# Kernel tuning notes

Measured on AMD Instinct MI355X. Metric: run time of the kernel, lower is better.

## Reference

```python
import jax, jax.numpy as jnp
import numpy as np

EPS = 1e-08
PARTIAL_NORM = 1.5
TOPK = 8
SELF_MOD_STEPS = 2


def _layernorm(x, g, b, eps=1e-05):
    mu = jnp.mean(x, axis=-1, keepdims=True)
    var = jnp.mean((x - mu) ** 2, axis=-1, keepdims=True)
    return (x - mu) / jnp.sqrt(var + eps) * g + b


def _spectral_normalize(w, iters=10):
    # mimic torch spectral_norm: divide by top singular value (power iteration)
    u = jnp.ones((w.shape[0],), w.dtype) / np.sqrt(w.shape[0])
    def step(u, _):
        v = w.T @ u
        v = v / (jnp.linalg.norm(v) + 1e-12)
        u2 = w @ v
        u2 = u2 / (jnp.linalg.norm(u2) + 1e-12)
        return u2, None
    u, _ = jax.lax.scan(step, u, None, length=iters)
    v = w.T @ u
    v = v / (jnp.linalg.norm(v) + 1e-12)
    sigma = u @ (w @ v)
    return w / sigma


def setup_inputs() -> dict:
    B, D, H, S, C = 8192, 2048, 1024, 3, 1000
    P = 1024  # proj_dim = ((max(H, D//2)+7)//8)*8
    key = jax.random.key(0)
    ks = jax.random.split(key, 16)
    x = jax.random.normal(ks[0], (B, D), jnp.float32)
    proj_w = jax.random.normal(ks[1], (P, D), jnp.float32) / np.sqrt(D)
    proj_b = jnp.zeros((P,), jnp.float32)
    ln_p_g = jnp.ones((P,), jnp.float32)
    ln_p_b = jnp.zeros((P,), jnp.float32)
    wf_w = jax.random.normal(ks[2], (S, 2 * H, P), jnp.float32) / np.sqrt(P)
    wf_w = jax.vmap(_spectral_normalize)(wf_w)
    wf_b = jax.random.normal(ks[3], (S, 2 * H), jnp.float32) * 0.02
    ln_g = jnp.ones((S, 2 * H), jnp.float32)
    ln_b = jnp.zeros((S, 2 * H), jnp.float32)
    temperature = jnp.ones((1,), jnp.float32)
    phases = jax.random.normal(ks[4], (S, 1), jnp.float32) * 0.5
    gate_w = jax.random.normal(ks[5], (H, H), jnp.float32) / np.sqrt(H)
    gate_b = jnp.zeros((H,), jnp.float32)
    cls_w1 = jax.random.normal(ks[6], (H, H), jnp.float32) / np.sqrt(H)
    cls_b1 = jnp.zeros((H,), jnp.float32)
    cls_w2 = jax.random.normal(ks[7], (C, H), jnp.float32) / np.sqrt(H)
    cls_b2 = jnp.zeros((C,), jnp.float32).at[1].set(0.75)
    return {"x": x, "proj_w": proj_w, "proj_b": proj_b, "ln_p_g": ln_p_g,
            "ln_p_b": ln_p_b, "wf_w": wf_w, "wf_b": wf_b, "ln_g": ln_g,
            "ln_b": ln_b, "temperature": temperature, "phases": phases,
            "gate_w": gate_w, "gate_b": gate_b, "cls_w1": cls_w1,
            "cls_b1": cls_b1, "cls_w2": cls_w2, "cls_b2": cls_b2}


def reference(x, proj_w, proj_b, ln_p_g, ln_p_b, wf_w, wf_b, ln_g, ln_b,
              temperature, phases, gate_w, gate_b, cls_w1, cls_b1, cls_w2, cls_b2):
    H = wf_w.shape[1] // 2
    # input projection (dropout is identity at eval)
    h = jax.nn.gelu(_layernorm(x @ proj_w.T + proj_b, ln_p_g, ln_p_b), approximate=False)
    # all wavefunctions at once: [B, S, 2H]
    out = jnp.einsum('bp,sep->bse', h, wf_w) + wf_b[None]
    out = _layernorm(out, ln_g[None], ln_b[None])
    out = jnp.exp(-out * out)  # ArcBell
    alpha, beta = out[..., :H], out[..., H:]
    norm_sq = jnp.sum(alpha ** 2 + beta ** 2, axis=-1, keepdims=True) + EPS
    factor = jnp.sqrt(PARTIAL_NORM ** 2 / norm_sq)
    alpha = alpha * factor
    beta = beta * factor
    phase = phases[None]  # [1, S, 1]
    c, s = jnp.cos(phase), jnp.sin(phase)
    wave_r = alpha * c - beta * s  # [B, S, H]
    wave_i = alpha * s + beta * c
    # cosine-similarity interference weights
    mean_real = jnp.mean(wave_r, axis=1)  # [B, H]
    mean_norm = jnp.sqrt(jnp.sum(mean_real ** 2, axis=-1, keepdims=True)) + EPS  # [B,1]
    wave_norms = jnp.sqrt(jnp.sum(wave_r ** 2, axis=-1, keepdims=True)) + EPS  # [B,S,1]
    dot = jnp.sum(wave_r * mean_real[:, None], axis=-1, keepdims=True)  # [B,S,1]
    cos_sim = (dot / (wave_norms * mean_norm[:, None]))[..., 0]  # [B,S]
    w = jax.nn.softmax(cos_sim / temperature, axis=1)[..., None]  # [B,S,1]
    sup_r = jnp.sum(wave_r * w, axis=1)  # [B,H]
    sup_i = jnp.sum(wave_i * w, axis=1)
    # self-modulation with leaky residual
    for _ in range(SELF_MOD_STEPS):
        mag = jnp.sqrt(sup_r ** 2 + sup_i ** 2 + EPS)
        gate = jax.nn.sigmoid(mag @ gate_w.T + gate_b)
        sup_r = sup_r * gate + sup_r * 0.1
        sup_i = sup_i * gate + sup_i * 0.1
    mag_sq = sup_r ** 2 + sup_i ** 2
    # top-k mask + scatter + renormalize
    _, inds = jax.lax.top_k(mag_sq, TOPK)
    rows = jnp.arange(mag_sq.shape[0])[:, None]
    mask = jnp.zeros_like(mag_sq).at[rows, inds].set(1.0)
    masked = mag_sq * mask
    probs = masked / (jnp.sum(masked, axis=-1, keepdims=True) + EPS)
    # classifier (dropout identity at eval)
    hid = jax.nn.gelu(probs @ cls_w1.T + cls_b1, approximate=False)
    logits = hid @ cls_w2.T + cls_b2
    return logits
```

## Files before the change

kernel.cpp:

```cpp
#include <hip/hip_runtime.h>
#include <cstdint>

typedef __attribute__((ext_vector_type(8))) __bf16 bf16x8;
typedef __attribute__((ext_vector_type(4))) __bf16 bf16x4;
typedef __attribute__((ext_vector_type(4))) float f32x4;
typedef unsigned long long u64;

__device__ __forceinline__ void gld_lds16(const void* g, void* l) {
  __builtin_amdgcn_global_load_lds(
      (const __attribute__((address_space(1))) void*)g,
      (__attribute__((address_space(3))) void*)l, 16, 0, 0);
}

__device__ __forceinline__ float block_sum(float v, float* scr) {
#pragma unroll
  for (int off = 32; off > 0; off >>= 1) v += __shfl_down(v, off, 64);
  const int w = threadIdx.x >> 6;
  __syncthreads();
  if ((threadIdx.x & 63) == 0) scr[w] = v;
  __syncthreads();
  float s = 0.f;
  const int nw = blockDim.x >> 6;
  for (int i = 0; i < nw; ++i) s += scr[i];
  return s;
}

__device__ __forceinline__ float gelu_fast(float x) {
  const float ax = fabsf(x) * 0.70710678118654752f;
  const float t = 1.f / (1.f + 0.3275911f * ax);
  const float e = __expf(-ax * ax);
  float poly = 1.061405429f;
  poly = poly * t - 1.453152027f;
  poly = poly * t + 1.421413741f;
  poly = poly * t - 0.284496736f;
  poly = poly * t + 0.254829592f;
  const float erfax = 1.f - poly * t * e;
  const float er = copysignf(erfax, x);
  return 0.5f * x * (1.f + er);
}

__global__ __launch_bounds__(256) void k_cast_bf16(const float* __restrict__ in,
                                                   __bf16* __restrict__ out) {
  const long i = ((long)blockIdx.x * 256 + threadIdx.x) * 4;
  f32x4 v = *(const f32x4*)(in + i);
  bf16x4 o = {(__bf16)v[0], (__bf16)v[1], (__bf16)v[2], (__bf16)v[3]};
  *(bf16x4*)(out + i) = o;
}

__global__ __launch_bounds__(256) void k_cast_weights(
    const float* __restrict__ pw, __bf16* __restrict__ w1b,
    const float* __restrict__ wfw, __bf16* __restrict__ wfwb,
    const float* __restrict__ gw, __bf16* __restrict__ gwb) {
  const int bid = blockIdx.x;
  const float* in;
  __bf16* out;
  long base;
  if (bid < 2048) { in = pw; out = w1b; base = (long)bid * 1024; }
  else if (bid < 8192) { in = wfw; out = wfwb; base = (long)(bid - 2048) * 1024; }
  else { in = gw; out = gwb; base = (long)(bid - 8192) * 1024; }
  const long i = base + threadIdx.x * 4;
  f32x4 v = *(const f32x4*)(in + i);
  bf16x4 o = {(__bf16)v[0], (__bf16)v[1], (__bf16)v[2], (__bf16)v[3]};
  *(bf16x4*)(out + i) = o;
}

__global__ __launch_bounds__(256) void k_cast_pad(const float* __restrict__ in,
                                                  __bf16* __restrict__ out,
                                                  int rows_real, int cols) {
  const long i = ((long)blockIdx.x * 256 + threadIdx.x) * 4;
  const int row = (int)(i / cols);
  const int col = (int)(i % cols);
  bf16x4 o;
  if (row < rows_real) {
    f32x4 v = *(const f32x4*)(in + (long)row * cols + col);
    o = (bf16x4){(__bf16)v[0], (__bf16)v[1], (__bf16)v[2], (__bf16)v[3]};
  } else {
    o = (bf16x4){(__bf16)0.f, (__bf16)0.f, (__bf16)0.f, (__bf16)0.f};
  }
  *(bf16x4*)(out + i) = o;
}

__global__ __launch_bounds__(256) void k_transpose1k(const float* __restrict__ in,
                                                     float* __restrict__ out) {
  __shared__ float t[32][33];
  const int tx = threadIdx.x & 31;
  const int ty = threadIdx.x >> 5;
  const int r0 = blockIdx.y * 32, c0 = blockIdx.x * 32;
#pragma unroll
  for (int k = 0; k < 4; ++k)
    t[ty + 8 * k][tx] = in[(long)(r0 + ty + 8 * k) * 1024 + c0 + tx];
  __syncthreads();
#pragma unroll
  for (int k = 0; k < 4; ++k)
    out[(long)(c0 + ty + 8 * k) * 1024 + r0 + tx] = t[tx][ty + 8 * k];
}

__global__ __launch_bounds__(512, 1) void k_gemm256_bt(
    const __bf16* __restrict__ A, const __bf16* __restrict__ B,
    const float* __restrict__ bias, __bf16* __restrict__ C,
    int M, int N, int K) {
  __shared__ __align__(16) __bf16 lds[2][2][256 * 64];
  const int tid = threadIdx.x;
  const int lane = tid & 63;
  const int wid = tid >> 6;
  const int wr = wid >> 2;
  const int wc = wid & 3;
  const int gx = gridDim.x, gy = gridDim.y;
  const int lin = blockIdx.y * gx + blockIdx.x;
  const int xcd = lin & 7;
  const int local = lin >> 3;
  const int byq = gy >> 3;
  const int bx = local / byq;
  const int by = xcd * byq + (local % byq);
  const int m0 = by * 256, n0 = bx * 256;
  const int fr = lane & 15;
  const int fx = lane >> 4;
  const int px = lane & 7;

  const __bf16* Abase = A + (long)m0 * K;
  const __bf16* Bbase = B + (long)n0 * K;

  auto stage_q = [&](int slot, int kt, int mat, int half) {
    const __bf16* src = (mat ? Bbase : Abase) + kt * 64;
#pragma unroll
    for (int q = 0; q < 2; ++q) {
      const int idx = q * 512 + tid;
      const int r = idx >> 3;
      const int pblk = idx & 7;
      const int row = half * 128 + r;
      const int lblk = pblk ^ (r & 7);
      gld_lds16(src + (long)row * K + lblk * 8,
                (char*)&lds[slot][mat][row * 64 + pblk * 8]);
    }
  };
  auto frag = [&](int slot, int mat, int row, int ks) -> bf16x8 {
    return *(const bf16x8*)&lds[slot][mat][row * 64 + ((((ks << 2) + fx) ^ px) << 3)];
  };

  f32x4 acc[8][4] = {};
  const int nt = K >> 6;
#pragma unroll
  for (int qp = 0; qp < 4; ++qp) stage_q(0, 0, qp >> 1, qp & 1);

  const int arow = wr * 128 + fr;
  const int brow = wc * 64 + fr;

  for (int t = 0; t < nt; ++t) {
    const int sc = t & 1, sn = sc ^ 1;
    if (t + 1 < nt) {
#pragma unroll
      for (int qp = 0; qp < 4; ++qp) stage_q(sn, t + 1, qp >> 1, qp & 1);
      asm volatile("s_waitcnt vmcnt(8)" ::: "memory");
    } else {
      asm volatile("s_waitcnt vmcnt(0)" ::: "memory");
    }
    __builtin_amdgcn_sched_barrier(0);
    __builtin_amdgcn_s_barrier();
    bf16x8 b0[4], b1[4];
#pragma unroll
    for (int j = 0; j < 4; ++j) {
      b0[j] = frag(sc, 1, brow + j * 16, 0);
      b1[j] = frag(sc, 1, brow + j * 16, 1);
    }
    __builtin_amdgcn_s_setprio(1);
#pragma unroll
    for (int im = 0; im < 8; ++im) {
      bf16x8 x0 = frag(sc, 0, arow + im * 16, 0);
      bf16x8 x1 = frag(sc, 0, arow + im * 16, 1);
#pragma unroll
      for (int j = 0; j < 4; ++j) {
        acc[im][j] = __builtin_amdgcn_mfma_f32_16x16x32_bf16(x0, b0[j], acc[im][j], 0, 0, 0);
        acc[im][j] = __builtin_amdgcn_mfma_f32_16x16x32_bf16(x1, b1[j], acc[im][j], 0, 0, 0);
      }
    }
    __builtin_amdgcn_s_setprio(0);
    __builtin_amdgcn_s_barrier();
  }

  __bf16* cb = (__bf16*)&lds[0][0][0];
  const int lm0 = wr * 128 + fx * 4;
  const int lc0 = wc * 64 + fr;
#pragma unroll
  for (int j = 0; j < 4; ++j) {
    const float bv = bias[n0 + lc0 + j * 16];
#pragma unroll
    for (int im = 0; im < 8; ++im)
#pragma unroll
      for (int r = 0; r < 4; ++r)
        cb[(lm0 + im * 16 + r) * 256 + lc0 + j * 16] = (__bf16)(acc[im][j][r] + bv);
  }
  __syncthreads();
#pragma unroll
  for (int q = 0; q < 16; ++q) {
    const int idx = q * 512 + tid;
    const int row = idx >> 5;
    const int c8 = (idx & 31) * 8;
    *(f32x4*)(C + (long)(m0 + row) * N + n0 + c8) = *(const f32x4*)(cb + row * 256 + c8);
  }
}

template <int EPI, int BM>
__global__ __launch_bounds__(256) void k_gemm_bt(
    const __bf16* __restrict__ A, const __bf16* __restrict__ B,
    const float* __restrict__ bias, void* __restrict__ Cout,
    int M, int N, int K, int Nreal,
    float* __restrict__ msq, __bf16* __restrict__ magOut) {
  constexpr int MR = BM / 32;
  constexpr int STAGE_B = (2 * BM * 32 + 2 * 128 * 32) * 2;
  constexpr int CB_B = BM * 64 * 4;
  constexpr int SMEM_B = STAGE_B > CB_B ? STAGE_B : CB_B;
  __shared__ __align__(16) char smem[SMEM_B];
  __bf16* As = (__bf16*)smem;
  __bf16* Bs = (__bf16*)(smem + (size_t)2 * BM * 32 * 2);
  float* cb = (float*)smem;
  const int tid = threadIdx.x;
  const int lane = tid & 63;
  const int wid = tid >> 6;
  const int wr = wid >> 1, wc = wid & 1;

  const int gx = gridDim.x, gy = gridDim.y;
  const int nwg = gx * gy;
  int bx, by;
  if ((nwg & 7) == 0) {
    const int lin = blockIdx.y * gx + blockIdx.x;
    const int cpx = nwg >> 3;
    const int w = (lin & 7) * cpx + (lin >> 3);
    bx = w / gy;
    by = w % gy;
  } else {
    bx = blockIdx.x;
    by = blockIdx.y;
  }
  const int m0 = by * BM;
  const int n0 = bx * 128;
  const int frow = lane & 15;
  const int fk = (lane >> 4) * 8;
  f32x4 acc[MR][4] = {};

  auto stage = [&](int buf, int k0) {
    const __bf16* Ab = A + (long)m0 * K + k0;
    const __bf16* Bb = B + (long)n0 * K + k0;
    __bf16* Asb = As + buf * BM * 32;
    __bf16* Bsb = Bs + buf * 128 * 32;
#pragma unroll
    for (int q = 0; q < BM / 64; ++q) {
      const int idx = q * 256 + tid;
      const int row = idx >> 2;
      const int col = (idx & 3) * 8;
      gld_lds16(Ab + (long)row * K + col, (char*)Asb + idx * 16);
    }
#pragma unroll
    for (int q = 0; q < 2; ++q) {
      const int idx = q * 256 + tid;
      const int row = idx >> 2;
      const int col = (idx & 3) * 8;
      gld_lds16(Bb + (long)row * K + col, (char*)Bsb + idx * 16);
    }
  };

  const int nt = K >> 5;
  int cur = 0;
  stage(0, 0);
  __syncthreads();
  for (int t = 0; t < nt; ++t) {
    if (t + 1 < nt) stage(cur ^ 1, (t + 1) << 5);
    bf16x8 af[MR], bfr[4];
#pragma unroll
    for (int i = 0; i < MR; ++i)
      af[i] = *(const bf16x8*)(As + cur * BM * 32 + (wr * (BM / 2) + i * 16 + frow) * 32 + fk);
#pragma unroll
    for (int i = 0; i < 4; ++i)
      bfr[i] = *(const bf16x8*)(Bs + cur * 128 * 32 + (wc * 64 + i * 16 + frow) * 32 + fk);
#pragma unroll
    for (int im = 0; im < MR; ++im)
#pragma unroll
      for (int in = 0; in < 4; ++in)
        acc[im][in] = __builtin_amdgcn_mfma_f32_16x16x32_bf16(af[im], bfr[in],
                                                              acc[im][in], 0, 0, 0);
    __syncthreads();
    cur ^= 1;
  }

  if (EPI == 0 || EPI == 6 || EPI == 7) {
#pragma unroll 1
    for (int h = 0; h < 2; ++h) {
      __syncthreads();
      if (wc == h) {
#pragma unroll
        for (int in = 0; in < 4; ++in) {
          const int col = n0 + h * 64 + in * 16 + frow;
          const float bv = (col < Nreal) ? bias[col] : 0.f;
          const int lcc = in * 16 + frow;
#pragma unroll
          for (int im = 0; im < MR; ++im)
#pragma unroll
            for (int r = 0; r < 4; ++r) {
              const float v = acc[im][in][r] + bv;
              float sv;
              if (EPI == 0) {
                sv = v;
              } else {
                const float f = 1.f / (1.f + __expf(-v)) + 0.1f;
                sv = f * f;
              }
              cb[(wr * (BM / 2) + (lane >> 4) * 4 + im * 16 + r) * 64 + lcc] = sv;
            }
        }
      }
      __syncthreads();
#pragma unroll
      for (int q = 0; q < BM / 16; ++q) {
        const int idx = q * 256 + tid;
        const int row = idx >> 4;
        const int c4 = (idx & 15) * 4;
        const int gc = n0 + h * 64 + c4;
        if (EPI == 0) {
          if (gc < Nreal)
            *(f32x4*)((float*)Cout + (long)(m0 + row) * Nreal + gc) =
                *(const f32x4*)(cb + row * 64 + c4);
        } else {
          const long gix = (long)(m0 + row) * Nreal + gc;
          f32x4 m = *(const f32x4*)(msq + gix);
          const f32x4 f2 = *(const f32x4*)(cb + row * 64 + c4);
          m[0] *= f2[0]; m[1] *= f2[1]; m[2] *= f2[2]; m[3] *= f2[3];
          *(f32x4*)(msq + gix) = m;
          if (EPI == 6) {
            bf16x4 mg = {(__bf16)sqrtf(m[0] + 1e-8f), (__bf16)sqrtf(m[1] + 1e-8f),
                         (__bf16)sqrtf(m[2] + 1e-8f), (__bf16)sqrtf(m[3] + 1e-8f)};
            *(bf16x4*)(magOut + gix) = mg;
          }
        }
      }
    }
  } else {
    const int crow0 = m0 + wr * (BM / 2) + (lane >> 4) * 4;
    const int ccol0 = n0 + wc * 64 + (lane & 15);
#pragma unroll
    for (int in = 0; in < 4; ++in) {
      const int col = ccol0 + in * 16;
      if (col >= Nreal) continue;
      const float bv = bias[col];
#pragma unroll
      for (int im = 0; im < MR; ++im) {
#pragma unroll
        for (int r = 0; r < 4; ++r) {
          const long row = crow0 + im * 16 + r;
          ((__bf16*)Cout)[row * Nreal + col] = (__bf16)(acc[im][in][r] + bv);
        }
      }
    }
  }
}

__global__ __launch_bounds__(256) void k_ln_gelu(const float* __restrict__ y,
                                                 const float* __restrict__ g,
                                                 const float* __restrict__ b,
                                                 __bf16* __restrict__ h) {
  __shared__ float scr[8];
  const int tid = threadIdx.x;
  const long row = blockIdx.x;
  const float* yr = y + row * 1024;
  f32x4 v = *(const f32x4*)(yr + tid * 4);
  float ls = v[0] + v[1] + v[2] + v[3];
  const float mu = block_sum(ls, scr) * (1.f / 1024.f);
  float lss = 0.f;
#pragma unroll
  for (int j = 0; j < 4; ++j) {
    const float d = v[j] - mu;
    lss += d * d;
  }
  const float var = block_sum(lss, scr) * (1.f / 1024.f);
  const float rstd = rsqrtf(var + 1e-5f);
  bf16x4 o;
#pragma unroll
  for (int j = 0; j < 4; ++j) {
    const int c = tid * 4 + j;
    const float t = (v[j] - mu) * rstd * g[c] + b[c];
    o[j] = (__bf16)gelu_fast(t);
  }
  *(bf16x4*)(h + row * 1024 + tid * 4) = o;
}

__global__ __launch_bounds__(256) void k_stage_c(
    const __bf16* __restrict__ outb, const float* __restrict__ ln_g,
    const float* __restrict__ ln_b, const float* __restrict__ phases,
    const float* __restrict__ temp, float* __restrict__ msq,
    __bf16* __restrict__ mag0, int b0) {
  __shared__ float wrs[3][1024];
  __shared__ float wis[3][1024];
  __shared__ float gbuf[2048];
  __shared__ float scr[8];
  const int tid = threadIdx.x;
  const long b = blockIdx.x;

#pragma unroll 1
  for (int s = 0; s < 3; ++s) {
    const __bf16* src = outb + b * 6144 + s * 2048;
    bf16x8 v8 = *(const bf16x8*)(src + tid * 8);
    float x[8];
#pragma unroll
    for (int j = 0; j < 8; ++j) x[j] = (float)v8[j];
    float ls = 0.f;
#pragma unroll
    for (int j = 0; j < 8; ++j) ls += x[j];
    const float mu = block_sum(ls, scr) * (1.f / 2048.f);
    float lss = 0.f;
#pragma unroll
    for (int j = 0; j < 8; ++j) {
      const float d = x[j] - mu;
      lss += d * d;
    }
    const float var = block_sum(lss, scr) * (1.f / 2048.f);
    const float rstd = rsqrtf(var + 1e-5f);
    const float* lg = ln_g + s * 2048;
    const float* lb = ln_b + s * 2048;
    float nsq = 0.f;
#pragma unroll
    for (int j = 0; j < 8; ++j) {
      const int e = tid * 8 + j;
      const float yv = (x[j] - mu) * rstd * lg[e] + lb[e];
      const float gv = __expf(-yv * yv);
      gbuf[e] = gv;
      nsq += gv * gv;
    }
    const float normsq = block_sum(nsq, scr) + 1e-8f;
    const float factor = sqrtf(2.25f / normsq);
    const float ph = phases[s];
    const float cs = cosf(ph), sn = sinf(ph);
#pragma unroll
    for (int j = 0; j < 4; ++j) {
      const int h = j * 256 + tid;
      const float a = gbuf[h] * factor;
      const float bb = gbuf[h + 1024] * factor;
      wrs[s][h] = a * cs - bb * sn;
      wis[s][h] = a * sn + bb * cs;
    }
    __syncthreads();
  }

  float mr[4];
  float pmn = 0.f;
#pragma unroll
  for (int j = 0; j < 4; ++j) {
    const int h = j * 256 + tid;
    const float m = (wrs[0][h] + wrs[1][h] + wrs[2][h]) * (1.f / 3.f);
    mr[j] = m;
    pmn += m * m;
  }
  const float mnorm = sqrtf(block_sum(pmn, scr)) + 1e-8f;
  float csim[3];
#pragma unroll 1
  for (int s = 0; s < 3; ++s) {
    float pd = 0.f, pw = 0.f;
#pragma unroll
    for (int j = 0; j < 4; ++j) {
      const int h = j * 256 + tid;
      const float w = wrs[s][h];
      pd += w * mr[j];
      pw += w * w;
    }
    const float dot = block_sum(pd, scr);
    const float wn = sqrtf(block_sum(pw, scr)) + 1e-8f;
    csim[s] = dot / (wn * mnorm);
  }
  const float T = temp[0];
  const float t0 = csim[0] / T, t1 = csim[1] / T, t2 = csim[2] / T;
  const float mx = fmaxf(t0, fmaxf(t1, t2));
  const float e0 = __expf(t0 - mx), e1 = __expf(t1 - mx), e2 = __expf(t2 - mx);
  const float inv = 1.f / (e0 + e1 + e2);
  const float w0 = e0 * inv, w1 = e1 * inv, w2 = e2 * inv;
#pragma unroll
  for (int j = 0; j < 4; ++j) {
    const int h = j * 256 + tid;
    const float sr = wrs[0][h] * w0 + wrs[1][h] * w1 + wrs[2][h] * w2;
    const float si = wis[0][h] * w0 + wis[1][h] * w1 + wis[2][h] * w2;
    const float m2 = sr * sr + si * si;
    msq[(long)(b0 + b) * 1024 + h] = m2;
    mag0[(long)(b0 + b) * 1024 + h] = (__bf16)sqrtf(m2 + 1e-8f);
  }
}

__global__ __launch_bounds__(256) void k_topk_cls1(
    const float* __restrict__ msq,
    const float* __restrict__ w1t, const float* __restrict__ b1,
    __bf16* __restrict__ hid) {
  __shared__ u64 candk[32];
  __shared__ u64 selk_s[8];
  __shared__ float ssum_s;
  const int tid = threadIdx.x;
  const int lane = tid & 63;
  const int wv = tid >> 6;
  const long b = blockIdx.x;

  f32x4 mv = *(const f32x4*)(msq + b * 1024 + tid * 4);
  u64 key[4];
#pragma unroll
  for (int j = 0; j < 4; ++j)
    key[j] = ((u64)__float_as_uint(mv[j]) << 32) | (unsigned)(~(unsigned)(tid * 4 + j));
  u64 lm = key[0];
  int jm = 0;
#pragma unroll
  for (int j = 1; j < 4; ++j)
    if (key[j] > lm) { lm = key[j]; jm = j; }

#pragma unroll 1
  for (int it = 0; it < 8; ++it) {
    u64 bk = lm;
#pragma unroll
    for (int m = 1; m < 64; m <<= 1) {
      const u64 ok = __shfl_xor(bk, m, 64);
      bk = ok > bk ? ok : bk;
    }
    if (lane == 0) candk[wv * 8 + it] = bk;
    if (bk == lm) {
      key[jm] = 0ULL;
      lm = key[0]; jm = 0;
#pragma unroll
      for (int j = 1; j < 4; ++j)
        if (key[j] > lm) { lm = key[j]; jm = j; }
    }
  }
  __syncthreads();

  if (wv == 0) {
    u64 ck = (lane < 32) ? candk[lane] : 0ULL;
    float ss = 0.f;
#pragma unroll 1
    for (int it = 0; it < 8; ++it) {
      u64 bk = ck;
#pragma unroll
      for (int m = 1; m < 64; m <<= 1) {
        const u64 ok = __shfl_xor(bk, m, 64);
        bk = ok > bk ? ok : bk;
      }
      if (ck == bk) ck = 0ULL;
      if (lane == 0) {
        selk_s[it] = bk;
        ss += __uint_as_float((unsigned)(bk >> 32));
      }
    }
    if (lane == 0) ssum_s = ss;
  }
  __syncthreads();

  const float denom = 1.f / (ssum_s + 1e-8f);
  float p[8];
  int idx[8];
#pragma unroll
  for (int k = 0; k < 8; ++k) {
    const u64 kk = selk_s[k];
    p[k] = __uint_as_float((unsigned)(kk >> 32)) * denom;
    idx[k] = (int)(~(unsigned)kk & 1023u);
  }

  const int o0 = tid * 4;
  float acc0 = b1[o0], acc1 = b1[o0 + 1], acc2 = b1[o0 + 2], acc3 = b1[o0 + 3];
#pragma unroll
  for (int k = 0; k < 8; ++k) {
    const f32x4 wrow = *(const f32x4*)(w1t + (long)idx[k] * 1024 + o0);
    acc0 += p[k] * wrow[0];
    acc1 += p[k] * wrow[1];
    acc2 += p[k] * wrow[2];
    acc3 += p[k] * wrow[3];
  }
  bf16x4 o = {(__bf16)gelu_fast(acc0), (__bf16)gelu_fast(acc1),
              (__bf16)gelu_fast(acc2), (__bf16)gelu_fast(acc3)};
  *(bf16x4*)(hid + b * 1024 + o0) = o;
}

extern "C" void kernel_launch(void* const* d_in, const int* in_sizes, int n_in,
                              void* d_out, int out_size, void* d_ws, size_t ws_size,
                              hipStream_t stream) {
  const float* x      = (const float*)d_in[0];
  const float* proj_w = (const float*)d_in[1];
  const float* proj_b = (const float*)d_in[2];
  const float* ln_p_g = (const float*)d_in[3];
  const float* ln_p_b = (const float*)d_in[4];
  const float* wf_w   = (const float*)d_in[5];
  const float* wf_b   = (const float*)d_in[6];
  const float* ln_g   = (const float*)d_in[7];
  const float* ln_b   = (const float*)d_in[8];
  const float* temperature = (const float*)d_in[9];
  const float* phases = (const float*)d_in[10];
  const float* gate_w = (const float*)d_in[11];
  const float* gate_b = (const float*)d_in[12];
  const float* cls_w1 = (const float*)d_in[13];
  const float* cls_b1 = (const float*)d_in[14];
  const float* cls_w2 = (const float*)d_in[15];
  const float* cls_b2 = (const float*)d_in[16];
  float* out = (float*)d_out;
  (void)in_sizes; (void)n_in; (void)out_size;

  char* ws = (char*)d_ws;
  const size_t MB = 1024 * 1024;

  if (ws_size >= 196 * MB) {
    __bf16* xb   = (__bf16*)(ws + 0);
    float*  msq  = (float*)(ws + 0);
    float*  y1   = (float*)(ws + 32 * MB);
    __bf16* mag0 = (__bf16*)(ws + 32 * MB);
    __bf16* mag1 = (__bf16*)(ws + 48 * MB);
    __bf16* outb = (__bf16*)(ws + 64 * MB);
    __bf16* hid  = (__bf16*)(ws + 64 * MB);
    float*  w1t  = (float*)(ws + 96 * MB);
    __bf16* hb   = (__bf16*)(ws + 160 * MB);
    __bf16* wfwb = (__bf16*)(ws + 176 * MB);
    __bf16* gwb  = (__bf16*)(ws + 188 * MB);
    __bf16* c2b  = (__bf16*)(ws + 190 * MB);
    __bf16* w1b  = (__bf16*)(ws + 192 * MB);

    k_cast_bf16<<<16384, 256, 0, stream>>>(x, xb);
    k_cast_weights<<<9216, 256, 0, stream>>>(proj_w, w1b, wf_w, wfwb, gate_w, gwb);
    k_cast_pad<<<1024, 256, 0, stream>>>(cls_w2, c2b, 1000, 1024);

    k_gemm_bt<0, 64><<<dim3(8, 128), 256, 0, stream>>>(xb, w1b, proj_b, y1, 8192, 1024, 2048, 1024, nullptr, nullptr);
    k_ln_gelu<<<8192, 256, 0, stream>>>(y1, ln_p_g, ln_p_b, hb);

    k_gemm256_bt<<<dim3(24, 32), 512, 0, stream>>>(hb, wfwb, wf_b, outb, 8192, 6144, 1024);
    k_stage_c<<<8192, 256, 0, stream>>>(outb, ln_g, ln_b, phases, temperature, msq, mag0, 0);

    k_transpose1k<<<dim3(32, 32), 256, 0, stream>>>(cls_w1, w1t);
    k_gemm_bt<6, 64><<<dim3(8, 128), 256, 0, stream>>>(mag0, gwb, gate_b, nullptr, 8192, 1024, 1024, 1024, msq, mag1);
    k_gemm_bt<7, 64><<<dim3(8, 128), 256, 0, stream>>>(mag1, gwb, gate_b, nullptr, 8192, 1024, 1024, 1024, msq, nullptr);

    k_topk_cls1<<<8192, 256, 0, stream>>>(msq, w1t, cls_b1, hid);
    k_gemm_bt<0, 64><<<dim3(8, 128), 256, 0, stream>>>(hid, c2b, cls_b2, out, 8192, 1024, 1024, 1000, nullptr, nullptr);
  } else {
    __bf16* xb   = (__bf16*)(ws + 0);
    float*  msq  = (float*)(ws + 0);
    float*  y1   = (float*)(ws + 32 * MB);
    __bf16* outc = (__bf16*)(ws + 32 * MB);
    __bf16* mag1 = (__bf16*)(ws + 32 * MB);
    __bf16* hid  = (__bf16*)(ws + 48 * MB);
    __bf16* w1b  = (__bf16*)(ws + 64 * MB);
    __bf16* mag0 = (__bf16*)(ws + 64 * MB);
    __bf16* wfwb = (__bf16*)(ws + 96 * MB);
    __bf16* hb   = (__bf16*)(ws + 108 * MB);
    float*  w1t  = (float*)(ws + 108 * MB);
    __bf16* gwb  = (__bf16*)(ws + 124 * MB);
    __bf16* c2b  = (__bf16*)(ws + 126 * MB);

    k_cast_bf16<<<16384, 256, 0, stream>>>(x, xb);
    k_cast_weights<<<9216, 256, 0, stream>>>(proj_w, w1b, wf_w, wfwb, gate_w, gwb);
    k_cast_pad<<<1024, 256, 0, stream>>>(cls_w2, c2b, 1000, 1024);

    k_gemm_bt<0, 64><<<dim3(8, 128), 256, 0, stream>>>(xb, w1b, proj_b, y1, 8192, 1024, 2048, 1024, nullptr, nullptr);
    k_ln_gelu<<<8192, 256, 0, stream>>>(y1, ln_p_g, ln_p_b, hb);

    for (int c = 0; c < 4; ++c) {
      k_gemm_bt<1, 128><<<dim3(48, 16), 256, 0, stream>>>(hb + (size_t)c * 2048 * 1024, wfwb, wf_b,
                                                          outc, 2048, 6144, 1024, 6144, nullptr, nullptr);
      k_stage_c<<<2048, 256, 0, stream>>>(outc, ln_g, ln_b, phases, temperature,
                                          msq, mag0, c * 2048);
    }

    k_transpose1k<<<dim3(32, 32), 256, 0, stream>>>(cls_w1, w1t);
    k_gemm_bt<6, 64><<<dim3(8, 128), 256, 0, stream>>>(mag0, gwb, gate_b, nullptr, 8192, 1024, 1024, 1024, msq, mag1);
    k_gemm_bt<7, 64><<<dim3(8, 128), 256, 0, stream>>>(mag1, gwb, gate_b, nullptr, 8192, 1024, 1024, 1024, msq, nullptr);

    k_topk_cls1<<<8192, 256, 0, stream>>>(msq, w1t, cls_b1, hid);
    k_gemm_bt<0, 64><<<dim3(8, 128), 256, 0, stream>>>(hid, c2b, cls_b2, out, 8192, 1024, 1024, 1000, nullptr, nullptr);
  }
}
```

Measured before the change: 500.6 us.

## Rewrite stage C as one wavefront per row with register-resident waves

The per-row wave/superposition kernel now uses a single 64-lane wavefront per batch row instead of 256 threads. All three wave vectors stay in registers and every reduction becomes a wavefront shuffle, which removes the shared-memory buffers and the many block-wide __syncthreads reductions. Mean and variance come from a single pass (E[x^2]-mu^2), and loads and stores are wider and vectorised. In exchange, register pressure per thread rises sharply and the single-pass variance is slightly less numerically robust.

```diff
diff --git a/kernel.cpp b/kernel.cpp
--- a/kernel.cpp
+++ b/kernel.cpp
@@ -381,102 +381,130 @@
   *(bf16x4*)(h + row * 1024 + tid * 4) = o;
 }
 
-__global__ __launch_bounds__(256) void k_stage_c(
+__global__ __launch_bounds__(64) void k_stage_c(
     const __bf16* __restrict__ outb, const float* __restrict__ ln_g,
     const float* __restrict__ ln_b, const float* __restrict__ phases,
     const float* __restrict__ temp, float* __restrict__ msq,
     __bf16* __restrict__ mag0, int b0) {
-  __shared__ float wrs[3][1024];
-  __shared__ float wis[3][1024];
-  __shared__ float gbuf[2048];
-  __shared__ float scr[8];
-  const int tid = threadIdx.x;
+  const int t = threadIdx.x;
   const long b = blockIdx.x;
+  float wr[3][16], wi[3][16];
 
 #pragma unroll 1
   for (int s = 0; s < 3; ++s) {
     const __bf16* src = outb + b * 6144 + s * 2048;
-    bf16x8 v8 = *(const bf16x8*)(src + tid * 8);
-    float x[8];
-#pragma unroll
-    for (int j = 0; j < 8; ++j) x[j] = (float)v8[j];
-    float ls = 0.f;
-#pragma unroll
-    for (int j = 0; j < 8; ++j) ls += x[j];
-    const float mu = block_sum(ls, scr) * (1.f / 2048.f);
-    float lss = 0.f;
+    const bf16x8 va0 = *(const bf16x8*)(src + t * 16);
+    const bf16x8 va1 = *(const bf16x8*)(src + t * 16 + 8);
+    const bf16x8 vb0 = *(const bf16x8*)(src + 1024 + t * 16);
+    const bf16x8 vb1 = *(const bf16x8*)(src + 1024 + t * 16 + 8);
+    float sum = 0.f, ssq = 0.f;
 #pragma unroll
     for (int j = 0; j < 8; ++j) {
-      const float d = x[j] - mu;
-      lss += d * d;
-    }
-    const float var = block_sum(lss, scr) * (1.f / 2048.f);
+      const float x0 = (float)va0[j], x1 = (float)va1[j];
+      const float x2 = (float)vb0[j], x3 = (float)vb1[j];
+      sum += x0 + x1 + x2 + x3;
+      ssq += x0 * x0 + x1 * x1 + x2 * x2 + x3 * x3;
+    }
+#pragma unroll
+    for (int m = 1; m < 64; m <<= 1) {
+      sum += __shfl_xor(sum, m, 64);
+      ssq += __shfl_xor(ssq, m, 64);
+    }
+    const float mu = sum * (1.f / 2048.f);
+    const float var = ssq * (1.f / 2048.f) - mu * mu;
     const float rstd = rsqrtf(var + 1e-5f);
+
     const float* lg = ln_g + s * 2048;
     const float* lb = ln_b + s * 2048;
+    float ag[16], bg[16];
     float nsq = 0.f;
 #pragma unroll
-    for (int j = 0; j < 8; ++j) {
-      const int e = tid * 8 + j;
-      const float yv = (x[j] - mu) * rstd * lg[e] + lb[e];
-      const float gv = __expf(-yv * yv);
-      gbuf[e] = gv;
-      nsq += gv * gv;
-    }
-    const float normsq = block_sum(nsq, scr) + 1e-8f;
-    const float factor = sqrtf(2.25f / normsq);
+    for (int c = 0; c < 4; ++c) {
+      const f32x4 ga = *(const f32x4*)(lg + t * 16 + c * 4);
+      const f32x4 ba = *(const f32x4*)(lb + t * 16 + c * 4);
+      const f32x4 gb = *(const f32x4*)(lg + 1024 + t * 16 + c * 4);
+      const f32x4 bb = *(const f32x4*)(lb + 1024 + t * 16 + c * 4);
+#pragma unroll
+      for (int j = 0; j < 4; ++j) {
+        const int e = c * 4 + j;
+        const float xa = (e < 8) ? (float)va0[e & 7] : (float)va1[e & 7];
+        const float xb = (e < 8) ? (float)vb0[e & 7] : (float)vb1[e & 7];
+        const float ya = (xa - mu) * rstd * ga[j] + ba[j];
+        const float yb = (xb - mu) * rstd * gb[j] + bb[j];
+        const float gva = __expf(-ya * ya);
+        const float gvb = __expf(-yb * yb);
+        ag[e] = gva;
+        bg[e] = gvb;
+        nsq += gva * gva + gvb * gvb;
+      }
+    }
+#pragma unroll
+    for (int m = 1; m < 64; m <<= 1) nsq += __shfl_xor(nsq, m, 64);
+    const float factor = sqrtf(2.25f / (nsq + 1e-8f));
     const float ph = phases[s];
-    const float cs = cosf(ph), sn = sinf(ph);
-#pragma unroll
-    for (int j = 0; j < 4; ++j) {
-      const int h = j * 256 + tid;
-      const float a = gbuf[h] * factor;
-      const float bb = gbuf[h + 1024] * factor;
-      wrs[s][h] = a * cs - bb * sn;
-      wis[s][h] = a * sn + bb * cs;
-    }
-    __syncthreads();
-  }
-
-  float mr[4];
+    const float cs = __cosf(ph), sn = __sinf(ph);
+#pragma unroll
+    for (int j = 0; j < 16; ++j) {
+      const float a = ag[j] * factor;
+      const float bb2 = bg[j] * factor;
+      wr[s][j] = a * cs - bb2 * sn;
+      wi[s][j] = a * sn + bb2 * cs;
+    }
+  }
+
+  float mr[16];
   float pmn = 0.f;
 #pragma unroll
-  for (int j = 0; j < 4; ++j) {
-    const int h = j * 256 + tid;
-    const float m = (wrs[0][h] + wrs[1][h] + wrs[2][h]) * (1.f / 3.f);
+  for (int j = 0; j < 16; ++j) {
+    const float m = (wr[0][j] + wr[1][j] + wr[2][j]) * (1.f / 3.f);
     mr[j] = m;
     pmn += m * m;
   }
-  const float mnorm = sqrtf(block_sum(pmn, scr)) + 1e-8f;
-  float csim[3];
-#pragma unroll 1
-  for (int s = 0; s < 3; ++s) {
-    float pd = 0.f, pw = 0.f;
-#pragma unroll
-    for (int j = 0; j < 4; ++j) {
-      const int h = j * 256 + tid;
-      const float w = wrs[s][h];
-      pd += w * mr[j];
-      pw += w * w;
-    }
-    const float dot = block_sum(pd, scr);
-    const float wn = sqrtf(block_sum(pw, scr)) + 1e-8f;
-    csim[s] = dot / (wn * mnorm);
+#pragma unroll
+  for (int m = 1; m < 64; m <<= 1) pmn += __shfl_xor(pmn, m, 64);
+  const float mnorm = sqrtf(pmn) + 1e-8f;
+
+  float pd0 = 0.f, pw0 = 0.f, pd1 = 0.f, pw1 = 0.f, pd2 = 0.f, pw2 = 0.f;
+#pragma unroll
+  for (int j = 0; j < 16; ++j) {
+    pd0 += wr[0][j] * mr[j]; pw0 += wr[0][j] * wr[0][j];
+    pd1 += wr[1][j] * mr[j]; pw1 += wr[1][j] * wr[1][j];
+    pd2 += wr[2][j] * mr[j]; pw2 += wr[2][j] * wr[2][j];
+  }
+#pragma unroll
+  for (int m = 1; m < 64; m <<= 1) {
+    pd0 += __shfl_xor(pd0, m, 64); pw0 += __shfl_xor(pw0, m, 64);
+    pd1 += __shfl_xor(pd1, m, 64); pw1 += __shfl_xor(pw1, m, 64);
+    pd2 += __shfl_xor(pd2, m, 64); pw2 += __shfl_xor(pw2, m, 64);
   }
   const float T = temp[0];
-  const float t0 = csim[0] / T, t1 = csim[1] / T, t2 = csim[2] / T;
-  const float mx = fmaxf(t0, fmaxf(t1, t2));
-  const float e0 = __expf(t0 - mx), e1 = __expf(t1 - mx), e2 = __expf(t2 - mx);
+  const float c0 = pd0 / ((sqrtf(pw0) + 1e-8f) * mnorm) / T;
+  const float c1 = pd1 / ((sqrtf(pw1) + 1e-8f) * mnorm) / T;
+  const float c2 = pd2 / ((sqrtf(pw2) + 1e-8f) * mnorm) / T;
+  const float mx = fmaxf(c0, fmaxf(c1, c2));
+  const float e0 = __expf(c0 - mx), e1 = __expf(c1 - mx), e2 = __expf(c2 - mx);
   const float inv = 1.f / (e0 + e1 + e2);
   const float w0 = e0 * inv, w1 = e1 * inv, w2 = e2 * inv;
-#pragma unroll
-  for (int j = 0; j < 4; ++j) {
-    const int h = j * 256 + tid;
-    const float sr = wrs[0][h] * w0 + wrs[1][h] * w1 + wrs[2][h] * w2;
-    const float si = wis[0][h] * w0 + wis[1][h] * w1 + wis[2][h] * w2;
-    const float m2 = sr * sr + si * si;
-    msq[(long)(b0 + b) * 1024 + h] = m2;
-    mag0[(long)(b0 + b) * 1024 + h] = (__bf16)sqrtf(m2 + 1e-8f);
+
+  const long base = (long)(b0 + b) * 1024 + t * 16;
+  float m2v[16];
+#pragma unroll
+  for (int j = 0; j < 16; ++j) {
+    const float sr = wr[0][j] * w0 + wr[1][j] * w1 + wr[2][j] * w2;
+    const float si = wi[0][j] * w0 + wi[1][j] * w1 + wi[2][j] * w2;
+    m2v[j] = sr * sr + si * si;
+  }
+#pragma unroll
+  for (int c = 0; c < 4; ++c) {
+    f32x4 o = {m2v[c * 4], m2v[c * 4 + 1], m2v[c * 4 + 2], m2v[c * 4 + 3]};
+    *(f32x4*)(msq + base + c * 4) = o;
+  }
+#pragma unroll
+  for (int c = 0; c < 2; ++c) {
+    bf16x8 o;
+#pragma unroll
+    for (int j = 0; j < 8; ++j) o[j] = (__bf16)sqrtf(m2v[c * 8 + j] + 1e-8f);
+    *(bf16x8*)(mag0 + base + c * 8) = o;
   }
 }
 
@@ -617,7 +645,7 @@
     k_ln_gelu<<<8192, 256, 0, stream>>>(y1, ln_p_g, ln_p_b, hb);
 
     k_gemm256_bt<<<dim3(24, 32), 512, 0, stream>>>(hb, wfwb, wf_b, outb, 8192, 6144, 1024);
-    k_stage_c<<<8192, 256, 0, stream>>>(outb, ln_g, ln_b, phases, temperature, msq, mag0, 0);
+    k_stage_c<<<8192, 64, 0, stream>>>(outb, ln_g, ln_b, phases, temperature, msq, mag0, 0);
 
     k_transpose1k<<<dim3(32, 32), 256, 0, stream>>>(cls_w1, w1t);
     k_gemm_bt<6, 64><<<dim3(8, 128), 256, 0, stream>>>(mag0, gwb, gate_b, nullptr, 8192, 1024, 1024, 1024, msq, mag1);
@@ -650,8 +678,8 @@
     for (int c = 0; c < 4; ++c) {
       k_gemm_bt<1, 128><<<dim3(48, 16), 256, 0, stream>>>(hb + (size_t)c * 2048 * 1024, wfwb, wf_b,
                                                           outc, 2048, 6144, 1024, 6144, nullptr, nullptr);
-      k_stage_c<<<2048, 256, 0, stream>>>(outc, ln_g, ln_b, phases, temperature,
-                                          msq, mag0, c * 2048);
+      k_stage_c<<<2048, 64, 0, stream>>>(outc, ln_g, ln_b, phases, temperature,
+                                         msq, mag0, c * 2048);
     }
 
     k_transpose1k<<<dim3(32, 32), 256, 0, stream>>>(cls_w1, w1t);
```

Measured after the change: 523.4 us. +4.6%, slower.
